# Kernel tuning notes

Hardware: AMD Instinct MI355X
Metric: run time of the kernel (lower is better)

## Reference

```python
import jax, jax.numpy as jnp
import numpy as np

B, IN, OUT = 131072, 256, 256
BITWIDTH = 7.0


def setup_inputs() -> dict:
    key = jax.random.key(0)
    k1, k2 = jax.random.split(key)
    # simulated int8 activations (integer-valued float32)
    act_in = jax.random.randint(k1, (B, IN), -127, 128).astype(jnp.float32)
    # UniformWeights: xavier_uniform then weight_quant to the int8 grid
    limit = float(np.sqrt(6.0 / (IN + OUT)))
    w = jax.random.uniform(k2, (OUT, IN), minval=-limit, maxval=limit, dtype=jnp.float32)
    w_range = jnp.max(jnp.abs(w))
    weight_exp = (jnp.ceil(jnp.log2(w_range)) - 7.0).astype(jnp.int32)
    weight = jnp.round(w / w_range * 127.0)  # int8-valued float32 [OUT, IN]
    return {"act_in": act_in, "exp_in": jnp.int32(0), "weight": weight, "weight_exp": weight_exp}


def _round_shift(x, shift):
    # RoundShift: floor-div by 2**shift, add floor(|remainder| / 2**(shift-1)), clip to int8
    two_s = jnp.exp2(shift)
    rt = jnp.floor(x / two_s)
    prob = jnp.abs(x - rt * two_s)
    dec = jnp.floor(prob / jnp.exp2(shift - 1.0))
    return jnp.clip(rt + dec, -127.0, 127.0)


def reference(act_in, exp_in, weight, weight_exp):
    # int8 GEMM simulated in fp32 (exact: |acc| < 2^24)
    temp = act_in @ weight.T  # [B, OUT] int32 accumulator values
    # RangeEstimate: full-tensor abs-max -> bitwidth
    r = jnp.max(jnp.abs(temp))
    bw = jnp.where(r > 0, jnp.ceil(jnp.log2(jnp.maximum(r, 1.0))), 0.0)
    shift = bw - BITWIDTH
    pos = shift > 0
    safe_shift = jnp.maximum(shift, 1.0)
    rounded = _round_shift(temp, safe_shift)
    act_out = jnp.where(pos, rounded, temp).astype(jnp.int8)
    exp_sum = jnp.asarray(exp_in, jnp.int32) + jnp.asarray(weight_exp, jnp.int32)
    exp_out = (exp_sum + jnp.where(pos, shift, 0.0).astype(jnp.int32)).astype(jnp.int16)
    return act_out, exp_out
```

## Files before the change

### kernel.cpp

```cpp
#include <hip/hip_runtime.h>
#include <stdint.h>


#define M_ROWS 131072
#define NK 256
#define TM 128
#define TILES 4
#define LSTR 272

typedef __attribute__((ext_vector_type(4))) int iv4;
typedef __attribute__((ext_vector_type(4))) float fv4;
typedef __attribute__((ext_vector_type(4))) unsigned int u32x4;

__device__ __forceinline__ iv4 mfma_i8(iv4 a, iv4 b, iv4 c) {
  asm("v_mfma_i32_16x16x64_i8 %0, %1, %2, %0" : "+v"(c) : "v"(a), "v"(b));
  return c;
}

__device__ __forceinline__ unsigned int pack_i8x4(float a, float b, float c,
                                                  float d) {
  return ((unsigned int)(int)a & 0xFFu) | (((unsigned int)(int)b & 0xFFu) << 8) |
         (((unsigned int)(int)c & 0xFFu) << 16) | ((unsigned int)(int)d << 24);
}

__global__ void wconv(const float* __restrict__ w, unsigned char* __restrict__ wi8,
                      int* __restrict__ gmax) {
  if (blockIdx.x == 0 && threadIdx.x == 0) *gmax = 0;
  const int i = blockIdx.x * 256 + threadIdx.x;
  const fv4 f = ((const fv4*)w)[i];
  ((unsigned int*)wi8)[i] = pack_i8x4(f.x, f.y, f.z, f.w);
}

__global__ __launch_bounds__(512, 1) void gemm_max_cvt(
    const float* __restrict__ act, const unsigned char* __restrict__ wi8,
    unsigned char* __restrict__ act8, int* __restrict__ gmax)
{
  __shared__ __align__(16) unsigned char As[TM * LSTR];
  __shared__ __align__(16) unsigned char Bs[NK * LSTR];
  __shared__ int smax;
  const int tid = threadIdx.x;
  if (tid == 0) smax = 0;

  for (int c = tid; c < NK * NK / 16; c += 512) {
    const int col = c >> 4, kc = (c & 15) << 4;
    *(u32x4*)&Bs[col * LSTR + kc] = *(const u32x4*)(wi8 + col * NK + kc);
  }

  const int lane = tid & 63;
  const int wave = tid >> 6;
  const int wr   = wave >> 2;
  const int wc   = wave & 3;
  const int lm   = lane & 15;
  const int lk   = lane >> 4;

  int imax = 0;

  for (int t = 0; t < TILES; ++t) {
    const int tb = blockIdx.x * (TILES * TM) + t * TM;

    __syncthreads();
#pragma unroll
    for (int j = 0; j < 4; ++j) {
      const int c   = j * 512 + tid;
      const int row = c >> 4;
      const int kc  = (c & 15) << 4;
      const float* p = act + (size_t)(tb + row) * NK + kc;
      const fv4 f0 = ((const fv4*)p)[0];
      const fv4 f1 = ((const fv4*)p)[1];
      const fv4 f2 = ((const fv4*)p)[2];
      const fv4 f3 = ((const fv4*)p)[3];
      u32x4 v;
      v.x = pack_i8x4(f0.x, f0.y, f0.z, f0.w);
      v.y = pack_i8x4(f1.x, f1.y, f1.z, f1.w);
      v.z = pack_i8x4(f2.x, f2.y, f2.z, f2.w);
      v.w = pack_i8x4(f3.x, f3.y, f3.z, f3.w);
      *(u32x4*)&As[row * LSTR + kc] = v;
      *(u32x4*)(act8 + (size_t)(tb + row) * NK + kc) = v;
    }
    __syncthreads();

    iv4 acc[4][4] = {};
#pragma unroll
    for (int kk = 0; kk < 4; ++kk) {
      iv4 af[4], bf[4];
#pragma unroll
      for (int mi = 0; mi < 4; ++mi)
        af[mi] = *(const iv4*)&As[(wr * 64 + mi * 16 + lm) * LSTR + kk * 64 + lk * 16];
#pragma unroll
      for (int ni = 0; ni < 4; ++ni)
        bf[ni] = *(const iv4*)&Bs[(wc * 64 + ni * 16 + lm) * LSTR + kk * 64 + lk * 16];
#pragma unroll
      for (int mi = 0; mi < 4; ++mi)
#pragma unroll
        for (int ni = 0; ni < 4; ++ni)
          acc[mi][ni] = mfma_i8(af[mi], bf[ni], acc[mi][ni]);
    }

#pragma unroll
    for (int mi = 0; mi < 4; ++mi)
#pragma unroll
      for (int ni = 0; ni < 4; ++ni)
#pragma unroll
        for (int r = 0; r < 4; ++r) {
          const int ti = acc[mi][ni][r];
          const int a = ti < 0 ? -ti : ti;
          imax = a > imax ? a : imax;
        }
  }

#pragma unroll
  for (int off = 32; off; off >>= 1) {
    const int o = __shfl_xor(imax, off, 64);
    imax = o > imax ? o : imax;
  }
  if (lane == 0) atomicMax(&smax, imax);
  __syncthreads();
  if (tid == 0) atomicMax(gmax, smax);
}

__global__ __launch_bounds__(512, 1) void gemm_quant(
    const unsigned char* __restrict__ act8, const unsigned char* __restrict__ wi8,
    int* __restrict__ out, const int* __restrict__ gmax,
    const int* __restrict__ exp_in, const int* __restrict__ wexp)
{
  __shared__ __align__(16) unsigned char As[TM * LSTR];
  __shared__ __align__(16) unsigned char Bs[NK * LSTR];

  const int rmax = *gmax;
  const int bw = (rmax <= 1) ? 0 : (32 - __clz(rmax - 1));
  const int shift = bw - 7;
  const bool pos = shift > 0;
  const int s = shift < 1 ? 1 : shift;

  const int tid = threadIdx.x;
  for (int c = tid; c < NK * NK / 16; c += 512) {
    const int col = c >> 4, kc = (c & 15) << 4;
    *(u32x4*)&Bs[col * LSTR + kc] = *(const u32x4*)(wi8 + col * NK + kc);
  }

  const int lane = tid & 63;
  const int wave = tid >> 6;
  const int wr   = wave >> 2;
  const int wc   = wave & 3;
  const int lm   = lane & 15;
  const int lk   = lane >> 4;

  for (int t = 0; t < TILES; ++t) {
    const int tb = blockIdx.x * (TILES * TM) + t * TM;

    __syncthreads();
#pragma unroll
    for (int j = 0; j < 4; ++j) {
      const int c   = j * 512 + tid;
      const int row = c >> 4;
      const int kc  = (c & 15) << 4;
      *(u32x4*)&As[row * LSTR + kc] =
          *(const u32x4*)(act8 + (size_t)(tb + row) * NK + kc);
    }
    __syncthreads();

    iv4 acc[4][4] = {};
#pragma unroll
    for (int kk = 0; kk < 4; ++kk) {
      iv4 af[4], bf[4];
#pragma unroll
      for (int mi = 0; mi < 4; ++mi)
        af[mi] = *(const iv4*)&As[(wr * 64 + mi * 16 + lm) * LSTR + kk * 64 + lk * 16];
#pragma unroll
      for (int ni = 0; ni < 4; ++ni)
        bf[ni] = *(const iv4*)&Bs[(wc * 64 + ni * 16 + lm) * LSTR + kk * 64 + lk * 16];
#pragma unroll
      for (int mi = 0; mi < 4; ++mi)
#pragma unroll
        for (int ni = 0; ni < 4; ++ni)
          acc[mi][ni] = mfma_i8(af[mi], bf[ni], acc[mi][ni]);
    }

#pragma unroll
    for (int mi = 0; mi < 4; ++mi)
#pragma unroll
      for (int ni = 0; ni < 4; ++ni)
#pragma unroll
        for (int r = 0; r < 4; ++r) {
          const int ti = acc[mi][ni][r];
          int q;
          if (pos) {
            const int rt = ti >> s;
            const int dec = (ti - (rt << s)) >> (s - 1);
            q = rt + dec;
            q = q > 127 ? 127 : (q < -127 ? -127 : q);
          } else {
            q = (int)(signed char)(ti & 0xFF);
          }
          const int m = tb + wr * 64 + mi * 16 + lk * 4 + r;
          const int n = wc * 64 + ni * 16 + lm;
          __builtin_nontemporal_store(q, &out[(size_t)m * NK + n]);
        }
  }

  if (blockIdx.x == 0 && tid == 0) {
    const int e = exp_in[0] + wexp[0] + (pos ? shift : 0);
    out[(size_t)M_ROWS * NK] = (int)(short)e;
  }
}

extern "C" void kernel_launch(void* const* d_in, const int* in_sizes, int n_in,
                              void* d_out, int out_size, void* d_ws, size_t ws_size,
                              hipStream_t stream) {
  const float* act   = (const float*)d_in[0];
  const int* exp_in  = (const int*)d_in[1];
  const float* wgt   = (const float*)d_in[2];
  const int* wexp    = (const int*)d_in[3];
  int* gmax           = (int*)d_ws;
  unsigned char* wi8  = (unsigned char*)d_ws + 4096;
  unsigned char* act8 = (unsigned char*)d_ws + (1 << 20);

  wconv<<<dim3(64), dim3(256), 0, stream>>>(wgt, wi8, gmax);
  gemm_max_cvt<<<dim3(M_ROWS / (TILES * TM)), dim3(512), 0, stream>>>(
      act, wi8, act8, gmax);
  gemm_quant<<<dim3(M_ROWS / (TILES * TM)), dim3(512), 0, stream>>>(
      act8, wi8, (int*)d_out, gmax, exp_in, wexp);
}
```

Before: 267.6 us.

## Split N across two blocks, shrink LDS, and read activations directly from global

Both GEMM kernels now split the 256 output columns into two halves, one per block, which doubles the grid and halves the weight tile held in shared memory. Launch bounds are raised to allow several blocks per CU. gemm_quant drops its activation shared-memory staging and loads A fragments straight from global memory. The aim is more resident waves to hide latency; the cost is that gemm_max_cvt re-reads and re-converts the fp32 activations in both column halves, and A loads in gemm_quant become strided global accesses.

```diff
diff --git a/kernel.cpp b/kernel.cpp
--- a/kernel.cpp
+++ b/kernel.cpp
@@ -5,6 +5,7 @@
 #define M_ROWS 131072
 #define NK 256
 #define TM 128
+#define TN 128
 #define TILES 4
 #define LSTR 272
 
@@ -31,19 +32,24 @@
   ((unsigned int*)wi8)[i] = pack_i8x4(f.x, f.y, f.z, f.w);
 }
 
-__global__ __launch_bounds__(512, 1) void gemm_max_cvt(
+__global__ __launch_bounds__(512, 4) void gemm_max_cvt(
     const float* __restrict__ act, const unsigned char* __restrict__ wi8,
     unsigned char* __restrict__ act8, int* __restrict__ gmax)
 {
   __shared__ __align__(16) unsigned char As[TM * LSTR];
-  __shared__ __align__(16) unsigned char Bs[NK * LSTR];
+  __shared__ __align__(16) unsigned char Bs[TN * LSTR];
   __shared__ int smax;
   const int tid = threadIdx.x;
   if (tid == 0) smax = 0;
 
-  for (int c = tid; c < NK * NK / 16; c += 512) {
+  const int bx = blockIdx.x;
+  const int ch = bx & 1;
+  const int rg = bx >> 1;
+
+  for (int c = tid; c < TN * NK / 16; c += 512) {
     const int col = c >> 4, kc = (c & 15) << 4;
-    *(u32x4*)&Bs[col * LSTR + kc] = *(const u32x4*)(wi8 + col * NK + kc);
+    *(u32x4*)&Bs[col * LSTR + kc] =
+        *(const u32x4*)(wi8 + (size_t)(ch * TN + col) * NK + kc);
   }
 
   const int lane = tid & 63;
@@ -56,7 +62,7 @@
   int imax = 0;
 
   for (int t = 0; t < TILES; ++t) {
-    const int tb = blockIdx.x * (TILES * TM) + t * TM;
+    const int tb = rg * (TILES * TM) + t * TM;
 
     __syncthreads();
 #pragma unroll
@@ -75,31 +81,32 @@
       v.z = pack_i8x4(f2.x, f2.y, f2.z, f2.w);
       v.w = pack_i8x4(f3.x, f3.y, f3.z, f3.w);
       *(u32x4*)&As[row * LSTR + kc] = v;
-      *(u32x4*)(act8 + (size_t)(tb + row) * NK + kc) = v;
+      if (ch == 0)
+        *(u32x4*)(act8 + (size_t)(tb + row) * NK + kc) = v;
     }
     __syncthreads();
 
-    iv4 acc[4][4] = {};
+    iv4 acc[4][2] = {};
 #pragma unroll
     for (int kk = 0; kk < 4; ++kk) {
-      iv4 af[4], bf[4];
+      iv4 af[4], bf[2];
 #pragma unroll
       for (int mi = 0; mi < 4; ++mi)
         af[mi] = *(const iv4*)&As[(wr * 64 + mi * 16 + lm) * LSTR + kk * 64 + lk * 16];
 #pragma unroll
-      for (int ni = 0; ni < 4; ++ni)
-        bf[ni] = *(const iv4*)&Bs[(wc * 64 + ni * 16 + lm) * LSTR + kk * 64 + lk * 16];
-#pragma unroll
-      for (int mi = 0; mi < 4; ++mi)
-#pragma unroll
-        for (int ni = 0; ni < 4; ++ni)
+      for (int ni = 0; ni < 2; ++ni)
+        bf[ni] = *(const iv4*)&Bs[(wc * 32 + ni * 16 + lm) * LSTR + kk * 64 + lk * 16];
+#pragma unroll
+      for (int mi = 0; mi < 4; ++mi)
+#pragma unroll
+        for (int ni = 0; ni < 2; ++ni)
           acc[mi][ni] = mfma_i8(af[mi], bf[ni], acc[mi][ni]);
     }
 
 #pragma unroll
     for (int mi = 0; mi < 4; ++mi)
 #pragma unroll
-      for (int ni = 0; ni < 4; ++ni)
+      for (int ni = 0; ni < 2; ++ni)
 #pragma unroll
         for (int r = 0; r < 4; ++r) {
           const int ti = acc[mi][ni][r];
@@ -118,13 +125,12 @@
   if (tid == 0) atomicMax(gmax, smax);
 }
 
-__global__ __launch_bounds__(512, 1) void gemm_quant(
+__global__ __launch_bounds__(512, 4) void gemm_quant(
     const unsigned char* __restrict__ act8, const unsigned char* __restrict__ wi8,
     int* __restrict__ out, const int* __restrict__ gmax,
     const int* __restrict__ exp_in, const int* __restrict__ wexp)
 {
-  __shared__ __align__(16) unsigned char As[TM * LSTR];
-  __shared__ __align__(16) unsigned char Bs[NK * LSTR];
+  __shared__ __align__(16) unsigned char Bs[TN * LSTR];
 
   const int rmax = *gmax;
   const int bw = (rmax <= 1) ? 0 : (32 - __clz(rmax - 1));
@@ -133,10 +139,16 @@
   const int s = shift < 1 ? 1 : shift;
 
   const int tid = threadIdx.x;
-  for (int c = tid; c < NK * NK / 16; c += 512) {
+  const int bx = blockIdx.x;
+  const int ch = bx & 1;
+  const int rg = bx >> 1;
+
+  for (int c = tid; c < TN * NK / 16; c += 512) {
     const int col = c >> 4, kc = (c & 15) << 4;
-    *(u32x4*)&Bs[col * LSTR + kc] = *(const u32x4*)(wi8 + col * NK + kc);
-  }
+    *(u32x4*)&Bs[col * LSTR + kc] =
+        *(const u32x4*)(wi8 + (size_t)(ch * TN + col) * NK + kc);
+  }
+  __syncthreads();
 
   const int lane = tid & 63;
   const int wave = tid >> 6;
@@ -146,40 +158,31 @@
   const int lk   = lane >> 4;
 
   for (int t = 0; t < TILES; ++t) {
-    const int tb = blockIdx.x * (TILES * TM) + t * TM;
-
-    __syncthreads();
-#pragma unroll
-    for (int j = 0; j < 4; ++j) {
-      const int c   = j * 512 + tid;
-      const int row = c >> 4;
-      const int kc  = (c & 15) << 4;
-      *(u32x4*)&As[row * LSTR + kc] =
-          *(const u32x4*)(act8 + (size_t)(tb + row) * NK + kc);
-    }
-    __syncthreads();
-
-    iv4 acc[4][4] = {};
+    const int tb = rg * (TILES * TM) + t * TM;
+    const unsigned char* arow =
+        act8 + (size_t)(tb + wr * 64 + lm) * NK + lk * 16;
+
+    iv4 acc[4][2] = {};
 #pragma unroll
     for (int kk = 0; kk < 4; ++kk) {
-      iv4 af[4], bf[4];
-#pragma unroll
-      for (int mi = 0; mi < 4; ++mi)
-        af[mi] = *(const iv4*)&As[(wr * 64 + mi * 16 + lm) * LSTR + kk * 64 + lk * 16];
-#pragma unroll
-      for (int ni = 0; ni < 4; ++ni)
-        bf[ni] = *(const iv4*)&Bs[(wc * 64 + ni * 16 + lm) * LSTR + kk * 64 + lk * 16];
-#pragma unroll
-      for (int mi = 0; mi < 4; ++mi)
-#pragma unroll
-        for (int ni = 0; ni < 4; ++ni)
+      iv4 af[4], bf[2];
+#pragma unroll
+      for (int mi = 0; mi < 4; ++mi)
+        af[mi] = *(const iv4*)(arow + (size_t)(mi * 16) * NK + kk * 64);
+#pragma unroll
+      for (int ni = 0; ni < 2; ++ni)
+        bf[ni] = *(const iv4*)&Bs[(wc * 32 + ni * 16 + lm) * LSTR + kk * 64 + lk * 16];
+#pragma unroll
+      for (int mi = 0; mi < 4; ++mi)
+#pragma unroll
+        for (int ni = 0; ni < 2; ++ni)
           acc[mi][ni] = mfma_i8(af[mi], bf[ni], acc[mi][ni]);
     }
 
 #pragma unroll
     for (int mi = 0; mi < 4; ++mi)
 #pragma unroll
-      for (int ni = 0; ni < 4; ++ni)
+      for (int ni = 0; ni < 2; ++ni)
 #pragma unroll
         for (int r = 0; r < 4; ++r) {
           const int ti = acc[mi][ni][r];
@@ -193,12 +196,12 @@
             q = (int)(signed char)(ti & 0xFF);
           }
           const int m = tb + wr * 64 + mi * 16 + lk * 4 + r;
-          const int n = wc * 64 + ni * 16 + lm;
+          const int n = ch * TN + wc * 32 + ni * 16 + lm;
           __builtin_nontemporal_store(q, &out[(size_t)m * NK + n]);
         }
   }
 
-  if (blockIdx.x == 0 && tid == 0) {
+  if (bx == 0 && tid == 0) {
     const int e = exp_in[0] + wexp[0] + (pos ? shift : 0);
     out[(size_t)M_ROWS * NK] = (int)(short)e;
   }
@@ -215,9 +218,9 @@
   unsigned char* wi8  = (unsigned char*)d_ws + 4096;
   unsigned char* act8 = (unsigned char*)d_ws + (1 << 20);
 
+  const int nblk = (M_ROWS / (TILES * TM)) * 2;
   wconv<<<dim3(64), dim3(256), 0, stream>>>(wgt, wi8, gmax);
-  gemm_max_cvt<<<dim3(M_ROWS / (TILES * TM)), dim3(512), 0, stream>>>(
-      act, wi8, act8, gmax);
-  gemm_quant<<<dim3(M_ROWS / (TILES * TM)), dim3(512), 0, stream>>>(
-      act8, wi8, (int*)d_out, gmax, exp_in, wexp);
-}
+  gemm_max_cvt<<<dim3(nblk), dim3(512), 0, stream>>>(act, wi8, act8, gmax);
+  gemm_quant<<<dim3(nblk), dim3(512), 0, stream>>>(act8, wi8, (int*)d_out,
+                                                   gmax, exp_in, wexp);
+}
```

Result: no change. 270.3 us (+1.0%).
